# Optimization experiments

Measured on AMD Instinct MI355X. Metric: run time of the kernel, lower is better.

Reference implementation:

```python
import jax, jax.numpy as jnp
import numpy as np

B, L, H = 32, 256, 384
MAX_WAVE = 2048  # config.max_wave_length


def setup_inputs() -> dict:
    key = jax.random.key(0)
    k1, k2 = jax.random.split(key)
    encoder_hidden_states = jax.random.normal(k1, (B, L, H), dtype=jnp.float32)
    durations_gt = jax.random.randint(k2, (B, L), 0, 15, dtype=jnp.int32)
    return {"encoder_hidden_states": encoder_hidden_states, "durations_gt": durations_gt}


def reference(encoder_hidden_states, durations_gt):
    # Length regulation: token i is repeated durations_gt[b, i] times along the
    # output frame axis; frames past the total length are zero-padded.
    csum = jnp.cumsum(durations_gt, axis=1)               # [B, L] inclusive cumsum
    total = csum[:, -1]                                    # [B] real lengths
    t = jnp.arange(MAX_WAVE, dtype=csum.dtype)             # [T]
    # frame t belongs to token idx where csum[idx-1] <= t < csum[idx]
    idx = jax.vmap(lambda c: jnp.searchsorted(c, t, side="right"))(csum)  # [B, T]
    valid = t[None, :] < total[:, None]                    # [B, T]
    safe_idx = jnp.clip(idx, 0, L - 1)
    gathered = jnp.take_along_axis(encoder_hidden_states, safe_idx[..., None], axis=1)  # [B, T, H]
    gathered = jnp.where(valid[..., None], gathered, 0.0)
    outputs = jnp.transpose(gathered, (0, 2, 1))           # [B, H, T] per custom-op output shape
    encoder_masks = valid.astype(encoder_hidden_states.dtype)  # [B, T]
    return outputs, encoder_masks
```

## Files before the change

kernel.cpp:

```cpp
#include <hip/hip_runtime.h>

constexpr int Lc = 256;
constexpr int Hc = 384;
constexpr int Tc = 2048;
constexpr int Bc = 32;
constexpr int T_PER_BLOCK = 1024;
constexpr int H_TILE = 16;
constexpr int PADW = 17;

typedef float  floatx4 __attribute__((ext_vector_type(4)));

__global__ __launch_bounds__(256) void lr_fused_kernel(
    const float* __restrict__ enc,
    const int*   __restrict__ dur,
    float*       __restrict__ out,
    float*       __restrict__ mask)
{
    const int tid  = threadIdx.x;
    const int lane = tid & 63;
    const int wv   = tid >> 6;
    const int b    = blockIdx.z;
    const int h0   = blockIdx.y * H_TILE;

    __shared__ float          s_enc[Lc * PADW];
    __shared__ unsigned short s_row[Tc];
    __shared__ int            s_wtot[4];

    const float* encb = enc + (size_t)b * (Lc * Hc) + h0;
    const int r  = tid >> 2;
    const int c4 = (tid & 3) * 4;
    floatx4 st[4];
#pragma unroll
    for (int it = 0; it < 4; ++it)
        st[it] = *reinterpret_cast<const floatx4*>(encb + (size_t)(r + it * 64) * Hc + c4);

    const int d = dur[b * Lc + tid];
    {
        uint4 f;
        f.x = 0x00FF00FFu; f.y = 0x00FF00FFu; f.z = 0x00FF00FFu; f.w = 0x00FF00FFu;
        *reinterpret_cast<uint4*>(s_row + tid * 8) = f;
    }

    int s = d;
#pragma unroll
    for (int off = 1; off < 64; off <<= 1) {
        int t = __shfl_up(s, off);
        if (lane >= off) s += t;
    }
    if (lane == 63) s_wtot[wv] = s;

#pragma unroll
    for (int it = 0; it < 4; ++it) {
        float* dst = s_enc + (r + it * 64) * PADW + c4;
        dst[0] = st[it].x; dst[1] = st[it].y; dst[2] = st[it].z; dst[3] = st[it].w;
    }

    __syncthreads();

    int pre = 0, total = 0;
#pragma unroll
    for (int w = 0; w < 4; ++w) {
        int t = s_wtot[w];
        total += t;
        if (w < wv) pre += t;
    }
    const int csum_i = s + pre;
    const int excl   = csum_i - d;
    int hiw = csum_i; if (hiw > Tc) hiw = Tc;
    for (int t = excl; t < hiw; ++t) s_row[t] = (unsigned short)tid;

    __syncthreads();

    const int tbase = blockIdx.x * T_PER_BLOCK + tid * 4;
    ushort4 iv = *reinterpret_cast<const ushort4*>(s_row + tbase);

    int   rowoff[4];
    float mflag[4];
    rowoff[0] = (int)iv.x * PADW; mflag[0] = (tbase + 0 < total) ? 1.0f : 0.0f;
    rowoff[1] = (int)iv.y * PADW; mflag[1] = (tbase + 1 < total) ? 1.0f : 0.0f;
    rowoff[2] = (int)iv.z * PADW; mflag[2] = (tbase + 2 < total) ? 1.0f : 0.0f;
    rowoff[3] = (int)iv.w * PADW; mflag[3] = (tbase + 3 < total) ? 1.0f : 0.0f;

    float* outb = out + (size_t)b * (Hc * Tc) + (size_t)h0 * Tc + tbase;
#pragma unroll
    for (int hh = 0; hh < H_TILE; ++hh) {
        floatx4 v;
        v.x = s_enc[rowoff[0] + hh] * mflag[0];
        v.y = s_enc[rowoff[1] + hh] * mflag[1];
        v.z = s_enc[rowoff[2] + hh] * mflag[2];
        v.w = s_enc[rowoff[3] + hh] * mflag[3];
        __builtin_nontemporal_store(v, reinterpret_cast<floatx4*>(outb + (size_t)hh * Tc));
    }

    if (blockIdx.y == 0) {
        floatx4 m;
        m.x = mflag[0]; m.y = mflag[1]; m.z = mflag[2]; m.w = mflag[3];
        __builtin_nontemporal_store(m, reinterpret_cast<floatx4*>(mask + (size_t)b * Tc + tbase));
    }
}

extern "C" void kernel_launch(void* const* d_in, const int* in_sizes, int n_in,
                              void* d_out, int out_size, void* d_ws, size_t ws_size,
                              hipStream_t stream) {
    const float* enc = (const float*)d_in[0];
    const int*   dur = (const int*)d_in[1];

    float* out  = (float*)d_out;
    float* mask = out + (size_t)Bc * Hc * Tc;

    dim3 grid(Tc / T_PER_BLOCK, Hc / H_TILE, Bc);
    dim3 block(256);
    lr_fused_kernel<<<grid, block, 0, stream>>>(enc, dur, out, mask);
}
```

Measured before the change: 26.96 us.

## Cover the full frame axis per block and vectorize shared-memory gathers

Each block now handles all 2048 frames for one batch and one H tile, using 512 threads instead of 256. Previously two blocks per tile each staged the same encoder tile and recomputed the same cumsum, so this removes that duplicated load and prefix-sum work. The shared-memory row pitch is padded to 20 floats so each thread can read four hidden values with one 16-byte LDS load instead of scalar loads. In exchange there are half as many blocks, each larger, and the wider padding may change LDS bank-conflict behaviour.

```diff
diff --git a/kernel.cpp b/kernel.cpp
--- a/kernel.cpp
+++ b/kernel.cpp
@@ -4,13 +4,12 @@
 constexpr int Hc = 384;
 constexpr int Tc = 2048;
 constexpr int Bc = 32;
-constexpr int T_PER_BLOCK = 1024;
 constexpr int H_TILE = 16;
-constexpr int PADW = 17;
+constexpr int PADW = 20;
 
-typedef float  floatx4 __attribute__((ext_vector_type(4)));
+typedef float floatx4 __attribute__((ext_vector_type(4)));
 
-__global__ __launch_bounds__(256) void lr_fused_kernel(
+__global__ __launch_bounds__(512) void lr_fused_kernel(
     const float* __restrict__ enc,
     const int*   __restrict__ dur,
     float*       __restrict__ out,
@@ -19,26 +18,26 @@
     const int tid  = threadIdx.x;
     const int lane = tid & 63;
     const int wv   = tid >> 6;
-    const int b    = blockIdx.z;
-    const int h0   = blockIdx.y * H_TILE;
+    const int b    = blockIdx.y;
+    const int h0   = blockIdx.x * H_TILE;
 
     __shared__ float          s_enc[Lc * PADW];
     __shared__ unsigned short s_row[Tc];
-    __shared__ int            s_wtot[4];
+    __shared__ int            s_wtot[8];
 
     const float* encb = enc + (size_t)b * (Lc * Hc) + h0;
     const int r  = tid >> 2;
     const int c4 = (tid & 3) * 4;
-    floatx4 st[4];
+    floatx4 st[2];
 #pragma unroll
-    for (int it = 0; it < 4; ++it)
-        st[it] = *reinterpret_cast<const floatx4*>(encb + (size_t)(r + it * 64) * Hc + c4);
+    for (int p = 0; p < 2; ++p)
+        st[p] = *reinterpret_cast<const floatx4*>(encb + (size_t)(r + p * 128) * Hc + c4);
 
-    const int d = dur[b * Lc + tid];
+    int d = 0;
+    if (tid < Lc) d = dur[b * Lc + tid];
     {
-        uint4 f;
-        f.x = 0x00FF00FFu; f.y = 0x00FF00FFu; f.z = 0x00FF00FFu; f.w = 0x00FF00FFu;
-        *reinterpret_cast<uint4*>(s_row + tid * 8) = f;
+        uint2 f; f.x = 0x00FF00FFu; f.y = 0x00FF00FFu;
+        *reinterpret_cast<uint2*>(s_row + tid * 4) = f;
     }
 
     int s = d;
@@ -50,9 +49,9 @@
     if (lane == 63) s_wtot[wv] = s;
 
 #pragma unroll
-    for (int it = 0; it < 4; ++it) {
-        float* dst = s_enc + (r + it * 64) * PADW + c4;
-        dst[0] = st[it].x; dst[1] = st[it].y; dst[2] = st[it].z; dst[3] = st[it].w;
+    for (int p = 0; p < 2; ++p) {
+        float* dst = s_enc + (r + p * 128) * PADW + c4;
+        dst[0] = st[p].x; dst[1] = st[p].y; dst[2] = st[p].z; dst[3] = st[p].w;
     }
 
     __syncthreads();
@@ -64,38 +63,50 @@
         total += t;
         if (w < wv) pre += t;
     }
-    const int csum_i = s + pre;
-    const int excl   = csum_i - d;
-    int hiw = csum_i; if (hiw > Tc) hiw = Tc;
-    for (int t = excl; t < hiw; ++t) s_row[t] = (unsigned short)tid;
+    if (tid < Lc) {
+        const int csum_i = s + pre;
+        const int excl   = csum_i - d;
+        int hiw = csum_i; if (hiw > Tc) hiw = Tc;
+        for (int t = excl; t < hiw; ++t) s_row[t] = (unsigned short)tid;
+    }
 
     __syncthreads();
 
-    const int tbase = blockIdx.x * T_PER_BLOCK + tid * 4;
+    const int tbase = tid * 4;
     ushort4 iv = *reinterpret_cast<const ushort4*>(s_row + tbase);
 
-    int   rowoff[4];
-    float mflag[4];
-    rowoff[0] = (int)iv.x * PADW; mflag[0] = (tbase + 0 < total) ? 1.0f : 0.0f;
-    rowoff[1] = (int)iv.y * PADW; mflag[1] = (tbase + 1 < total) ? 1.0f : 0.0f;
-    rowoff[2] = (int)iv.z * PADW; mflag[2] = (tbase + 2 < total) ? 1.0f : 0.0f;
-    rowoff[3] = (int)iv.w * PADW; mflag[3] = (tbase + 3 < total) ? 1.0f : 0.0f;
+    const int rowoff0 = (int)iv.x * PADW;
+    const int rowoff1 = (int)iv.y * PADW;
+    const int rowoff2 = (int)iv.z * PADW;
+    const int rowoff3 = (int)iv.w * PADW;
+    const float m0 = (tbase + 0 < total) ? 1.0f : 0.0f;
+    const float m1 = (tbase + 1 < total) ? 1.0f : 0.0f;
+    const float m2 = (tbase + 2 < total) ? 1.0f : 0.0f;
+    const float m3 = (tbase + 3 < total) ? 1.0f : 0.0f;
 
     float* outb = out + (size_t)b * (Hc * Tc) + (size_t)h0 * Tc + tbase;
 #pragma unroll
-    for (int hh = 0; hh < H_TILE; ++hh) {
-        floatx4 v;
-        v.x = s_enc[rowoff[0] + hh] * mflag[0];
-        v.y = s_enc[rowoff[1] + hh] * mflag[1];
-        v.z = s_enc[rowoff[2] + hh] * mflag[2];
-        v.w = s_enc[rowoff[3] + hh] * mflag[3];
-        __builtin_nontemporal_store(v, reinterpret_cast<floatx4*>(outb + (size_t)hh * Tc));
+    for (int hh0 = 0; hh0 < H_TILE; hh0 += 4) {
+        floatx4 a0 = *reinterpret_cast<const floatx4*>(s_enc + rowoff0 + hh0);
+        floatx4 a1 = *reinterpret_cast<const floatx4*>(s_enc + rowoff1 + hh0);
+        floatx4 a2 = *reinterpret_cast<const floatx4*>(s_enc + rowoff2 + hh0);
+        floatx4 a3 = *reinterpret_cast<const floatx4*>(s_enc + rowoff3 + hh0);
+#pragma unroll
+        for (int j = 0; j < 4; ++j) {
+            floatx4 v;
+            v.x = a0[j] * m0;
+            v.y = a1[j] * m1;
+            v.z = a2[j] * m2;
+            v.w = a3[j] * m3;
+            __builtin_nontemporal_store(
+                v, reinterpret_cast<floatx4*>(outb + (size_t)(hh0 + j) * Tc));
+        }
     }
 
-    if (blockIdx.y == 0) {
-        floatx4 m;
-        m.x = mflag[0]; m.y = mflag[1]; m.z = mflag[2]; m.w = mflag[3];
-        __builtin_nontemporal_store(m, reinterpret_cast<floatx4*>(mask + (size_t)b * Tc + tbase));
+    if (blockIdx.x == 0) {
+        floatx4 m; m.x = m0; m.y = m1; m.z = m2; m.w = m3;
+        __builtin_nontemporal_store(
+            m, reinterpret_cast<floatx4*>(mask + (size_t)b * Tc + tbase));
     }
 }
 
@@ -108,7 +119,7 @@
     float* out  = (float*)d_out;
     float* mask = out + (size_t)Bc * Hc * Tc;
 
-    dim3 grid(Tc / T_PER_BLOCK, Hc / H_TILE, Bc);
-    dim3 block(256);
+    dim3 grid(Hc / H_TILE, Bc);
+    dim3 block(512);
     lr_fused_kernel<<<grid, block, 0, stream>>>(enc, dur, out, mask);
 }
```

After: 24.11 us. -10.6%, faster.
